# Kernel tuning notes

Hardware: AMD Instinct MI355X
Metric: run time of the kernel (lower is better)

## Reference

```python
import jax, jax.numpy as jnp
import numpy as np

D_MODEL = 512
NHEAD = 8
D_K = D_MODEL // NHEAD


def setup_inputs() -> dict:
    key = jax.random.key(0)
    ks = jax.random.split(key, 7)
    B, L = 4, 2048
    x = jax.random.normal(ks[0], (B, L, D_MODEL), dtype=jnp.float32)
    scale = 1.0 / np.sqrt(D_MODEL)
    Wq = jax.random.normal(ks[1], (D_MODEL, D_MODEL), dtype=jnp.float32) * scale
    Wk = jax.random.normal(ks[2], (D_MODEL, D_MODEL), dtype=jnp.float32) * scale
    Wv = jax.random.normal(ks[3], (D_MODEL, D_MODEL), dtype=jnp.float32) * scale
    Wo = jax.random.normal(ks[4], (D_MODEL, D_MODEL), dtype=jnp.float32) * scale
    wave_freq = jax.random.normal(ks[5], (NHEAD,), dtype=jnp.float32) * 0.1
    wave_phase = jnp.zeros((NHEAD,), dtype=jnp.float32)
    return {"x": x, "Wq": Wq, "Wk": Wk, "Wv": Wv, "Wo": Wo,
            "wave_freq": wave_freq, "wave_phase": wave_phase}


def reference(x, Wq, Wk, Wv, Wo, wave_freq, wave_phase):
    B, L, D = x.shape
    H, dk = NHEAD, D_K
    # nn.Linear(bias=False): y = x @ W.T
    q = (x @ Wq.T).reshape(B, L, H, dk).transpose(0, 2, 1, 3)  # (B,H,L,dk)
    k = (x @ Wk.T).reshape(B, L, H, dk).transpose(0, 2, 1, 3)
    v = (x @ Wv.T).reshape(B, L, H, dk).transpose(0, 2, 1, 3)
    pos = jnp.arange(L, dtype=x.dtype)  # (L,)
    two_pi = jnp.asarray(2.0 * np.pi, dtype=x.dtype)
    # wave: (H, L) -> broadcast as (1, H, 1, L) over key positions
    wave = jnp.cos(two_pi * wave_freq[:, None] * pos[None, :] + wave_phase[:, None])
    scores = jnp.einsum('bhqd,bhkd->bhqk', q, k) * (dk ** -0.5)
    scores = scores * wave[None, :, None, :]
    attn = jax.nn.softmax(scores, axis=-1)
    out = jnp.einsum('bhqk,bhkd->bhqd', attn, v)
    out = out.transpose(0, 2, 1, 3).reshape(B, L, D)
    return out @ Wo.T
```

## Files before the change

### kernel.cpp

```cpp
#include <hip/hip_runtime.h>
#include <math.h>

#define D_MODEL 512
#define NHEAD   8
#define DK      64
#define BATCH   4
#define SEQ     2048
#define MTOT    (BATCH*SEQ)
#define NXELEM  (MTOT*D_MODEL)
#define NWELEM  (4*D_MODEL*D_MODEL)

typedef _Float16 half8   __attribute__((ext_vector_type(8)));
typedef _Float16 half4_t __attribute__((ext_vector_type(4)));
typedef __fp16   fp16x2  __attribute__((ext_vector_type(2)));
typedef float    f32x4   __attribute__((ext_vector_type(4)));

#define MFMA32(a,b,c) __builtin_amdgcn_mfma_f32_16x16x32_f16((a),(b),(c),0,0,0)

#define WSCALE 0.18033688011117130f

__global__ __launch_bounds__(256) void cvt_kernel(
    const float* __restrict__ x,
    const float* __restrict__ Wq, const float* __restrict__ Wk,
    const float* __restrict__ Wv, const float* __restrict__ Wo,
    const float* __restrict__ wf, const float* __restrict__ wp,
    _Float16* __restrict__ Xh, _Float16* __restrict__ Wh,
    float* __restrict__ wtab)
{
    const int tid = blockIdx.x * 256 + threadIdx.x;
    int idx = tid * 4;
    if (idx < NXELEM + NWELEM) {
        const float* src; _Float16* dst; int off;
        if (idx < NXELEM) { src = x; dst = Xh; off = idx; }
        else {
            int r = idx - NXELEM;
            int sel = r >> 18;
            off = r & ((1 << 18) - 1);
            src = (sel == 0) ? Wq : (sel == 1) ? Wk : (sel == 2) ? Wv : Wo;
            dst = Wh + ((size_t)sel << 18);
        }
        float4 v = *(const float4*)(src + off);
        half4_t h;
        h[0] = (_Float16)v.x; h[1] = (_Float16)v.y;
        h[2] = (_Float16)v.z; h[3] = (_Float16)v.w;
        *(half4_t*)(dst + off) = h;
    } else {
        int widx = idx - (NXELEM + NWELEM);
        const int h = widx >> 11;
        const int pos0 = widx & 2047;
        const float f  = 6.28318530717958647692f * wf[h];
        const float ph = wp[h];
        float4 o;
        o.x = WSCALE * cosf(fmaf(f, (float)(pos0 + 0), ph));
        o.y = WSCALE * cosf(fmaf(f, (float)(pos0 + 1), ph));
        o.z = WSCALE * cosf(fmaf(f, (float)(pos0 + 2), ph));
        o.w = WSCALE * cosf(fmaf(f, (float)(pos0 + 3), ph));
        *(float4*)(wtab + widx) = o;
    }
}

__global__ __launch_bounds__(256) void qkv_mfma_kernel(
    const _Float16* __restrict__ Xh, const _Float16* __restrict__ Wh,
    const float* __restrict__ wtab,
    _Float16* __restrict__ Qh, _Float16* __restrict__ Kh,
    _Float16* __restrict__ Vth)
{
    __shared__ _Float16 As[128][72];
    __shared__ _Float16 Bs[192][72];

    const int t  = threadIdx.x;
    const int h  = blockIdx.x;
    const int m0 = blockIdx.y * 128;

    const int w = t >> 6, lane = t & 63, ln = lane & 15, quad = lane >> 4;
    const int ar = t >> 1, ac = (t & 1) * 32;
    const int br = t >> 2, bc = (t & 3) * 16;

    const _Float16* ag  = Xh + (size_t)(m0 + ar) * 512 + ac;
    const _Float16* bg0 = Wh + (size_t)(h * 64 + br) * 512 + bc;
    const _Float16* bg1 = bg0 + (1 << 18);
    const _Float16* bg2 = bg0 + (2 << 18);

    const f32x4 kZero = {0.f, 0.f, 0.f, 0.f};
    f32x4 acc[3][2][4];
    #pragma unroll
    for (int c = 0; c < 3; ++c)
        #pragma unroll
        for (int i = 0; i < 2; ++i)
            #pragma unroll
            for (int j = 0; j < 4; ++j) acc[c][i][j] = kZero;

    for (int k0 = 0; k0 < 512; k0 += 64) {
        half8 av[4], bv[6];
        #pragma unroll
        for (int i = 0; i < 4; ++i) av[i] = *(const half8*)(ag + k0 + i * 8);
        bv[0] = *(const half8*)(bg0 + k0);
        bv[1] = *(const half8*)(bg0 + k0 + 8);
        bv[2] = *(const half8*)(bg1 + k0);
        bv[3] = *(const half8*)(bg1 + k0 + 8);
        bv[4] = *(const half8*)(bg2 + k0);
        bv[5] = *(const half8*)(bg2 + k0 + 8);
        __syncthreads();
        #pragma unroll
        for (int i = 0; i < 4; ++i) *(half8*)&As[ar][ac + i * 8] = av[i];
        #pragma unroll
        for (int c = 0; c < 3; ++c) {
            *(half8*)&Bs[c * 64 + br][bc]     = bv[2 * c];
            *(half8*)&Bs[c * 64 + br][bc + 8] = bv[2 * c + 1];
        }
        __syncthreads();

        #pragma unroll
        for (int ks = 0; ks < 2; ++ks) {
            half8 af[2];
            #pragma unroll
            for (int mt = 0; mt < 2; ++mt)
                af[mt] = *(const half8*)&As[w * 32 + mt * 16 + ln][ks * 32 + quad * 8];
            #pragma unroll
            for (int c = 0; c < 3; ++c) {
                half8 bf[4];
                #pragma unroll
                for (int nt = 0; nt < 4; ++nt)
                    bf[nt] = *(const half8*)&Bs[c * 64 + nt * 16 + ln][ks * 32 + quad * 8];
                #pragma unroll
                for (int mt = 0; mt < 2; ++mt)
                    #pragma unroll
                    for (int nt = 0; nt < 4; ++nt)
                        acc[c][mt][nt] = MFMA32(af[mt], bf[nt], acc[c][mt][nt]);
            }
        }
    }

    const int b  = m0 >> 11;
    const int l0 = m0 & 2047;
    const float* wt = wtab + h * SEQ;

    #pragma unroll
    for (int which = 0; which < 2; ++which) {
        _Float16* dst = (which == 0 ? Qh : Kh) + (size_t)(b * NHEAD + h) * SEQ * DK;
        __syncthreads();
        _Float16* Ql = &As[0][0];
        #pragma unroll
        for (int mt = 0; mt < 2; ++mt)
            #pragma unroll
            for (int r = 0; r < 4; ++r) {
                const int lr = w * 32 + mt * 16 + quad * 4 + r;
                const float wv = (which == 1) ? wt[l0 + lr] : 1.0f;
                #pragma unroll
                for (int nt = 0; nt < 4; ++nt)
                    Ql[lr * 72 + nt * 16 + ln] = (_Float16)(acc[which][mt][nt][r] * wv);
            }
        __syncthreads();
        #pragma unroll
        for (int rr = 0; rr < 4; ++rr) {
            const int row = rr * 32 + (t >> 3);
            half8 v = *(const half8*)&Ql[row * 72 + (t & 7) * 8];
            *(half8*)(dst + (size_t)(l0 + row) * DK + (t & 7) * 8) = v;
        }
    }

    __syncthreads();
    _Float16* Vl = &As[0][0];
    #pragma unroll
    for (int nt = 0; nt < 4; ++nt) {
        half8 hv;
        #pragma unroll
        for (int mt = 0; mt < 2; ++mt)
            #pragma unroll
            for (int r = 0; r < 4; ++r)
                hv[mt * 4 + r] = (_Float16)acc[2][mt][nt][r];
        const int d = nt * 16 + ln;
        *(half8*)&Vl[d * 136 + w * 32 + quad * 8] = hv;
    }
    __syncthreads();
    _Float16* dst = Vth + (size_t)(b * NHEAD + h) * DK * SEQ;
    #pragma unroll
    for (int rr = 0; rr < 4; ++rr) {
        const int d = rr * 16 + (t >> 4);
        half8 v = *(const half8*)&Vl[d * 136 + (t & 15) * 8];
        *(half8*)(dst + (size_t)d * SEQ + l0 + (t & 15) * 8) = v;
    }
}

__global__ __launch_bounds__(512, 4) void attn_mfma_kernel(
    const _Float16* __restrict__ Qh, const _Float16* __restrict__ Kwh,
    const _Float16* __restrict__ Vth, _Float16* __restrict__ AOh)
{
    __shared__ _Float16 SM[2][4][64][72];

    const int bx = blockIdx.x;
    const int g8 = bx & 7;
    const int s  = bx >> 3;
    const int bh = g8 * 4 + (s >> 4);
    const int q0 = (s & 15) * 128;
    const int b = bh >> 3, h = bh & 7;

    const int t = threadIdx.x;
    const int w = t >> 6;
    const int wg = w & 3;
    const int half = w >> 2;
    const int lane = t & 63, ln = lane & 15, quad = lane >> 4;

    const _Float16* Qg = Qh + ((size_t)bh * SEQ + q0) * DK;
    const _Float16* Kg = Kwh + (size_t)bh * SEQ * DK;
    const _Float16* Vg = Vth + (size_t)bh * DK * SEQ;
    const int kbase = half * 1024;

    const int tl = t & 255;
    const int sr = tl >> 2, sc = (tl & 3) * 16;
    const int qr = t >> 2, qc = (t & 3) * 16;

    {
        const _Float16* qp = Qg + (size_t)qr * DK + qc;
        half8 qv0 = *(const half8*)(qp);
        half8 qv1 = *(const half8*)(qp + 8);
        const _Float16* kp = Kg + (size_t)(kbase + sr) * DK + sc;
        const _Float16* vp = Vg + (size_t)sr * SEQ + kbase + sc;
        half8 kv0 = *(const half8*)(kp);
        half8 kv1 = *(const half8*)(kp + 8);
        half8 vv0 = *(const half8*)(vp);
        half8 vv1 = *(const half8*)(vp + 8);
        _Float16* qd = &SM[1][2 + (qr >> 6)][qr & 63][qc];
        *(half8*)(qd)     = qv0;
        *(half8*)(qd + 8) = qv1;
        *(half8*)&SM[half][0][sr][sc]     = kv0;
        *(half8*)&SM[half][0][sr][sc + 8] = kv1;
        *(half8*)&SM[half][1][sr][sc]     = vv0;
        *(half8*)&SM[half][1][sr][sc + 8] = vv1;
    }
    __syncthreads();

    half8 qf[2][2];
    #pragma unroll
    for (int u = 0; u < 2; ++u) {
        const int row = wg * 32 + u * 16 + ln;
        const _Float16* qsrc = &SM[1][2 + (row >> 6)][row & 63][0];
        qf[u][0] = *(const half8*)(qsrc + quad * 8);
        qf[u][1] = *(const half8*)(qsrc + 32 + quad * 8);
    }

    const f32x4 kZero = {0.f, 0.f, 0.f, 0.f};
    f32x4 o[2][4];
    #pragma unroll
    for (int u = 0; u < 2; ++u)
        #pragma unroll
        for (int nt = 0; nt < 4; ++nt) o[u][nt] = kZero;
    float l_acc[2] = {0.f, 0.f};

    for (int kt = 0; kt < 16; ++kt) {
        const int cur = kt & 1;

        half8 pk0, pk1, pv0, pv1;
        const bool more = (kt + 1 < 16);
        if (more) {
            const _Float16* kp = Kg + (size_t)(kbase + (kt + 1) * 64 + sr) * DK + sc;
            const _Float16* vp = Vg + (size_t)sr * SEQ + kbase + (kt + 1) * 64 + sc;
            pk0 = *(const half8*)(kp);
            pk1 = *(const half8*)(kp + 8);
            pv0 = *(const half8*)(vp);
            pv1 = *(const half8*)(vp + 8);
        }

        const _Float16 (*Ks)[72] = SM[half][2 * cur];
        const _Float16 (*Vs)[72] = SM[half][2 * cur + 1];

        #pragma unroll
        for (int g = 0; g < 2; ++g) {
            half8 ka0 = *(const half8*)&Ks[(2 * g + 0) * 16 + ln][quad * 8];
            half8 ka1 = *(const half8*)&Ks[(2 * g + 0) * 16 + ln][32 + quad * 8];
            half8 kb0 = *(const half8*)&Ks[(2 * g + 1) * 16 + ln][quad * 8];
            half8 kb1 = *(const half8*)&Ks[(2 * g + 1) * 16 + ln][32 + quad * 8];
            half8 vf[4];
            #pragma unroll
            for (int nt = 0; nt < 4; ++nt)
                vf[nt] = *(const half8*)&Vs[nt * 16 + ln][g * 32 + quad * 8];

            #pragma unroll
            for (int u = 0; u < 2; ++u) {
                f32x4 s0 = MFMA32(ka0, qf[u][0], kZero);
                f32x4 s1 = MFMA32(kb0, qf[u][0], kZero);
                s0 = MFMA32(ka1, qf[u][1], s0);
                s1 = MFMA32(kb1, qf[u][1], s1);

                const float e00 = __builtin_amdgcn_exp2f(s0[0]);
                const float e01 = __builtin_amdgcn_exp2f(s0[1]);
                const float e02 = __builtin_amdgcn_exp2f(s0[2]);
                const float e03 = __builtin_amdgcn_exp2f(s0[3]);
                const float e10 = __builtin_amdgcn_exp2f(s1[0]);
                const float e11 = __builtin_amdgcn_exp2f(s1[1]);
                const float e12 = __builtin_amdgcn_exp2f(s1[2]);
                const float e13 = __builtin_amdgcn_exp2f(s1[3]);
                union { half8 v; fp16x2 h2[4]; } pu;
                pu.h2[0] = __builtin_amdgcn_cvt_pkrtz(e00, e01);
                pu.h2[1] = __builtin_amdgcn_cvt_pkrtz(e02, e03);
                pu.h2[2] = __builtin_amdgcn_cvt_pkrtz(e10, e11);
                pu.h2[3] = __builtin_amdgcn_cvt_pkrtz(e12, e13);
                l_acc[u] += ((e00 + e01) + (e02 + e03)) + ((e10 + e11) + (e12 + e13));

                #pragma unroll
                for (int nt = 0; nt < 4; ++nt)
                    o[u][nt] = MFMA32(pu.v, vf[nt], o[u][nt]);
            }
        }

        __syncthreads();
        if (more) {
            _Float16* kd = &SM[half][2 * (cur ^ 1)][sr][sc];
            _Float16* vd = &SM[half][2 * (cur ^ 1) + 1][sr][sc];
            *(half8*)(kd)     = pk0;
            *(half8*)(kd + 8) = pk1;
            *(half8*)(vd)     = pv0;
            *(half8*)(vd + 8) = pv1;
        }
        __syncthreads();
    }

    float* OP = (float*)&SM[0][0][0][0];
    const int idx = wg * 64 + lane;
    if (half == 1) {
        #pragma unroll
        for (int u = 0; u < 2; ++u)
            #pragma unroll
            for (int nt = 0; nt < 4; ++nt)
                #pragma unroll
                for (int r = 0; r < 4; ++r)
                    OP[((u * 4 + nt) * 4 + r) * 257 + idx] = o[u][nt][r];
        OP[32 * 257 + idx] = l_acc[0];
        OP[33 * 257 + idx] = l_acc[1];
    }
    __syncthreads();
    if (half == 0) {
        #pragma unroll
        for (int u = 0; u < 2; ++u)
            #pragma unroll
            for (int nt = 0; nt < 4; ++nt)
                #pragma unroll
                for (int r = 0; r < 4; ++r)
                    o[u][nt][r] += OP[((u * 4 + nt) * 4 + r) * 257 + idx];
        l_acc[0] += OP[32 * 257 + idx];
        l_acc[1] += OP[33 * 257 + idx];

        #pragma unroll
        for (int u = 0; u < 2; ++u) {
            l_acc[u] += __shfl_xor(l_acc[u], 16);
            l_acc[u] += __shfl_xor(l_acc[u], 32);
        }

        #pragma unroll
        for (int u = 0; u < 2; ++u)
            #pragma unroll
            for (int r = 0; r < 4; ++r) {
                const float lr  = __shfl(l_acc[u], quad * 4 + r, 16);
                const float inv = 1.0f / lr;
                const int lq = q0 + wg * 32 + u * 16 + quad * 4 + r;
                const size_t base = ((size_t)b * SEQ + lq) * D_MODEL + h * DK;
                #pragma unroll
                for (int nt = 0; nt < 4; ++nt)
                    AOh[base + nt * 16 + ln] = (_Float16)(o[u][nt][r] * inv);
            }
    }
}

__global__ __launch_bounds__(256) void out_mfma_kernel(
    const _Float16* __restrict__ AOh, const _Float16* __restrict__ Woh,
    float* __restrict__ out)
{
    __shared__ _Float16 As[128][72];
    __shared__ _Float16 Bs[64][72];

    const int t  = threadIdx.x;
    const int n0 = blockIdx.x * 64;
    const int m0 = blockIdx.y * 128;

    const int w = t >> 6, lane = t & 63, ln = lane & 15, quad = lane >> 4;
    const int ar = t >> 1, ac = (t & 1) * 32;
    const int br = t >> 2, bc = (t & 3) * 16;

    const _Float16* ag = AOh + (size_t)(m0 + ar) * 512 + ac;
    const _Float16* bg = Woh + (size_t)(n0 + br) * 512 + bc;

    const f32x4 kZero = {0.f, 0.f, 0.f, 0.f};
    f32x4 acc[2][4];
    #pragma unroll
    for (int i = 0; i < 2; ++i)
        #pragma unroll
        for (int j = 0; j < 4; ++j) acc[i][j] = kZero;

    for (int k0 = 0; k0 < 512; k0 += 64) {
        half8 av[4], bv[2];
        #pragma unroll
        for (int i = 0; i < 4; ++i) av[i] = *(const half8*)(ag + k0 + i * 8);
        #pragma unroll
        for (int i = 0; i < 2; ++i) bv[i] = *(const half8*)(bg + k0 + i * 8);
        __syncthreads();
        #pragma unroll
        for (int i = 0; i < 4; ++i) *(half8*)&As[ar][ac + i * 8] = av[i];
        #pragma unroll
        for (int i = 0; i < 2; ++i) *(half8*)&Bs[br][bc + i * 8] = bv[i];
        __syncthreads();

        #pragma unroll
        for (int ks = 0; ks < 2; ++ks) {
            half8 af[2], bf[4];
            #pragma unroll
            for (int mt = 0; mt < 2; ++mt)
                af[mt] = *(const half8*)&As[w * 32 + mt * 16 + ln][ks * 32 + quad * 8];
            #pragma unroll
            for (int nt = 0; nt < 4; ++nt)
                bf[nt] = *(const half8*)&Bs[nt * 16 + ln][ks * 32 + quad * 8];
            #pragma unroll
            for (int mt = 0; mt < 2; ++mt)
                #pragma unroll
                for (int nt = 0; nt < 4; ++nt)
                    acc[mt][nt] = MFMA32(af[mt], bf[nt], acc[mt][nt]);
        }
    }

    float* Os = (float*)&As[0][0];
    #pragma unroll
    for (int pass = 0; pass < 2; ++pass) {
        __syncthreads();
        if ((w >> 1) == pass) {
            const int rbase = (w & 1) * 32;
            #pragma unroll
            for (int mt = 0; mt < 2; ++mt)
                #pragma unroll
                for (int r = 0; r < 4; ++r) {
                    const int row = rbase + mt * 16 + quad * 4 + r;
                    #pragma unroll
                    for (int nt = 0; nt < 4; ++nt)
                        Os[row * 66 + nt * 16 + ln] = acc[mt][nt][r];
                }
        }
        __syncthreads();
        #pragma unroll
        for (int rr = 0; rr < 4; ++rr) {
            const int row = rr * 16 + (t >> 4);
            float4 v = *(const float4*)&Os[row * 66 + (t & 15) * 4];
            *(float4*)(out + (size_t)(m0 + pass * 64 + row) * 512 + n0 + (t & 15) * 4) = v;
        }
    }
}

extern "C" void kernel_launch(void* const* d_in, const int* in_sizes, int n_in,
                              void* d_out, int out_size, void* d_ws, size_t ws_size,
                              hipStream_t stream)
{
    (void)in_sizes; (void)n_in; (void)out_size; (void)ws_size;
    const float* x  = (const float*)d_in[0];
    const float* Wq = (const float*)d_in[1];
    const float* Wk = (const float*)d_in[2];
    const float* Wv = (const float*)d_in[3];
    const float* Wo = (const float*)d_in[4];
    const float* wf = (const float*)d_in[5];
    const float* wp = (const float*)d_in[6];
    float* out = (float*)d_out;

    const size_t NX = (size_t)MTOT * D_MODEL;
    _Float16* Xh  = (_Float16*)d_ws;
    _Float16* Wh  = Xh + NX;
    _Float16* Qh  = Wh + 4 * 262144;
    _Float16* Kh  = Qh + NX;
    _Float16* Vth = Kh + NX;
    _Float16* AOh = Vth + NX;
    float*    wtab = (float*)(AOh + NX);

    cvt_kernel<<<5136, 256, 0, stream>>>(x, Wq, Wk, Wv, Wo, wf, wp, Xh, Wh, wtab);

    dim3 g1(8, 64);
    qkv_mfma_kernel<<<g1, 256, 0, stream>>>(Xh, Wh, wtab, Qh, Kh, Vth);

    attn_mfma_kernel<<<512, 512, 0, stream>>>(Qh, Kh, Vth, AOh);

    dim3 g3(8, 64);
    out_mfma_kernel<<<g3, 256, 0, stream>>>(AOh, Wh + 3 * 262144, out);
}
```

Before: 155.7 us.

## Halve attention block to 256 threads with 64 query rows per wave

Attention blocks shrink from 8 to 4 waves. Each wave now owns 64 query rows instead of 32, and K/V tiles are 32 keys per step over 32 steps instead of 64 keys over 16 steps. The aim is more register-level reuse of each K/V fragment across query subtiles, and less shared memory per block so more blocks fit per CU. In exchange each wave needs more accumulator registers, which may cut occupancy, and there are twice as many loop iterations with two barriers each.

```diff
diff --git a/kernel.cpp b/kernel.cpp
--- a/kernel.cpp
+++ b/kernel.cpp
@@ -182,11 +182,15 @@
     }
 }
 
-__global__ __launch_bounds__(512, 4) void attn_mfma_kernel(
+#define KOFF(h,b) ((b) * 9728 + (h) * 4864)
+#define VOFF(h,b) (KOFF(h,b) + 2304)
+#define QOFF      9728
+
+__global__ __launch_bounds__(256) void attn_mfma_kernel(
     const _Float16* __restrict__ Qh, const _Float16* __restrict__ Kwh,
     const _Float16* __restrict__ Vth, _Float16* __restrict__ AOh)
 {
-    __shared__ _Float16 SM[2][4][64][72];
+    __shared__ _Float16 SMEM[19456];
 
     const int bx = blockIdx.x;
     const int g8 = bx & 7;
@@ -197,116 +201,120 @@
 
     const int t = threadIdx.x;
     const int w = t >> 6;
-    const int wg = w & 3;
-    const int half = w >> 2;
+    const int wg = w & 1;
+    const int ch = w >> 1;
     const int lane = t & 63, ln = lane & 15, quad = lane >> 4;
 
     const _Float16* Qg = Qh + ((size_t)bh * SEQ + q0) * DK;
     const _Float16* Kg = Kwh + (size_t)bh * SEQ * DK;
     const _Float16* Vg = Vth + (size_t)bh * DK * SEQ;
-    const int kbase = half * 1024;
-
-    const int tl = t & 255;
-    const int sr = tl >> 2, sc = (tl & 3) * 16;
-    const int qr = t >> 2, qc = (t & 3) * 16;
+    const int kbase = (t >> 7) * 1024;
+
+    const int tl  = t & 127;
+    const int skr = tl >> 2, skc = (tl & 3) * 16;
+    const int svr = tl >> 1, svc = (tl & 1) * 16;
 
     {
+        const int qr = t >> 1, qc = (t & 1) * 32;
         const _Float16* qp = Qg + (size_t)qr * DK + qc;
-        half8 qv0 = *(const half8*)(qp);
-        half8 qv1 = *(const half8*)(qp + 8);
-        const _Float16* kp = Kg + (size_t)(kbase + sr) * DK + sc;
-        const _Float16* vp = Vg + (size_t)sr * SEQ + kbase + sc;
+        half8 q0v = *(const half8*)(qp);
+        half8 q1v = *(const half8*)(qp + 8);
+        half8 q2v = *(const half8*)(qp + 16);
+        half8 q3v = *(const half8*)(qp + 24);
+        const _Float16* kp = Kg + (size_t)(kbase + skr) * DK + skc;
+        const _Float16* vp = Vg + (size_t)svr * SEQ + kbase + svc;
         half8 kv0 = *(const half8*)(kp);
         half8 kv1 = *(const half8*)(kp + 8);
         half8 vv0 = *(const half8*)(vp);
         half8 vv1 = *(const half8*)(vp + 8);
-        _Float16* qd = &SM[1][2 + (qr >> 6)][qr & 63][qc];
-        *(half8*)(qd)     = qv0;
-        *(half8*)(qd + 8) = qv1;
-        *(half8*)&SM[half][0][sr][sc]     = kv0;
-        *(half8*)&SM[half][0][sr][sc + 8] = kv1;
-        *(half8*)&SM[half][1][sr][sc]     = vv0;
-        *(half8*)&SM[half][1][sr][sc + 8] = vv1;
+        _Float16* qd = &SMEM[QOFF + qr * 64 + qc];
+        *(half8*)(qd)      = q0v;
+        *(half8*)(qd + 8)  = q1v;
+        *(half8*)(qd + 16) = q2v;
+        *(half8*)(qd + 24) = q3v;
+        _Float16* kd = &SMEM[KOFF(t >> 7, 0) + skr * 72 + skc];
+        _Float16* vd = &SMEM[VOFF(t >> 7, 0) + svr * 40 + svc];
+        *(half8*)(kd)     = kv0;
+        *(half8*)(kd + 8) = kv1;
+        *(half8*)(vd)     = vv0;
+        *(half8*)(vd + 8) = vv1;
     }
     __syncthreads();
 
-    half8 qf[2][2];
-    #pragma unroll
-    for (int u = 0; u < 2; ++u) {
-        const int row = wg * 32 + u * 16 + ln;
-        const _Float16* qsrc = &SM[1][2 + (row >> 6)][row & 63][0];
+    half8 qf[4][2];
+    #pragma unroll
+    for (int u = 0; u < 4; ++u) {
+        const _Float16* qsrc = &SMEM[QOFF + (wg * 64 + u * 16 + ln) * 64];
         qf[u][0] = *(const half8*)(qsrc + quad * 8);
         qf[u][1] = *(const half8*)(qsrc + 32 + quad * 8);
     }
+    __syncthreads();
 
     const f32x4 kZero = {0.f, 0.f, 0.f, 0.f};
-    f32x4 o[2][4];
-    #pragma unroll
-    for (int u = 0; u < 2; ++u)
+    f32x4 o[4][4];
+    #pragma unroll
+    for (int u = 0; u < 4; ++u)
         #pragma unroll
         for (int nt = 0; nt < 4; ++nt) o[u][nt] = kZero;
-    float l_acc[2] = {0.f, 0.f};
-
-    for (int kt = 0; kt < 16; ++kt) {
+    float l_acc[4] = {0.f, 0.f, 0.f, 0.f};
+
+    for (int kt = 0; kt < 32; ++kt) {
         const int cur = kt & 1;
 
         half8 pk0, pk1, pv0, pv1;
-        const bool more = (kt + 1 < 16);
+        const bool more = (kt + 1 < 32);
         if (more) {
-            const _Float16* kp = Kg + (size_t)(kbase + (kt + 1) * 64 + sr) * DK + sc;
-            const _Float16* vp = Vg + (size_t)sr * SEQ + kbase + (kt + 1) * 64 + sc;
+            const _Float16* kp = Kg + (size_t)(kbase + (kt + 1) * 32 + skr) * DK + skc;
+            const _Float16* vp = Vg + (size_t)svr * SEQ + kbase + (kt + 1) * 32 + svc;
             pk0 = *(const half8*)(kp);
             pk1 = *(const half8*)(kp + 8);
             pv0 = *(const half8*)(vp);
             pv1 = *(const half8*)(vp + 8);
         }
 
-        const _Float16 (*Ks)[72] = SM[half][2 * cur];
-        const _Float16 (*Vs)[72] = SM[half][2 * cur + 1];
-
-        #pragma unroll
-        for (int g = 0; g < 2; ++g) {
-            half8 ka0 = *(const half8*)&Ks[(2 * g + 0) * 16 + ln][quad * 8];
-            half8 ka1 = *(const half8*)&Ks[(2 * g + 0) * 16 + ln][32 + quad * 8];
-            half8 kb0 = *(const half8*)&Ks[(2 * g + 1) * 16 + ln][quad * 8];
-            half8 kb1 = *(const half8*)&Ks[(2 * g + 1) * 16 + ln][32 + quad * 8];
-            half8 vf[4];
+        const _Float16* Ks = &SMEM[KOFF(ch, cur)];
+        const _Float16* Vs = &SMEM[VOFF(ch, cur)];
+
+        half8 ka0 = *(const half8*)&Ks[(ln)      * 72 + quad * 8];
+        half8 ka1 = *(const half8*)&Ks[(ln)      * 72 + 32 + quad * 8];
+        half8 kb0 = *(const half8*)&Ks[(16 + ln) * 72 + quad * 8];
+        half8 kb1 = *(const half8*)&Ks[(16 + ln) * 72 + 32 + quad * 8];
+        half8 vf[4];
+        #pragma unroll
+        for (int nt = 0; nt < 4; ++nt)
+            vf[nt] = *(const half8*)&Vs[(nt * 16 + ln) * 40 + quad * 8];
+
+        #pragma unroll
+        for (int u = 0; u < 4; ++u) {
+            f32x4 s0 = MFMA32(ka0, qf[u][0], kZero);
+            f32x4 s1 = MFMA32(kb0, qf[u][0], kZero);
+            s0 = MFMA32(ka1, qf[u][1], s0);
+            s1 = MFMA32(kb1, qf[u][1], s1);
+
+            const float e00 = __builtin_amdgcn_exp2f(s0[0]);
+            const float e01 = __builtin_amdgcn_exp2f(s0[1]);
+            const float e02 = __builtin_amdgcn_exp2f(s0[2]);
+            const float e03 = __builtin_amdgcn_exp2f(s0[3]);
+            const float e10 = __builtin_amdgcn_exp2f(s1[0]);
+            const float e11 = __builtin_amdgcn_exp2f(s1[1]);
+            const float e12 = __builtin_amdgcn_exp2f(s1[2]);
+            const float e13 = __builtin_amdgcn_exp2f(s1[3]);
+            union { half8 v; fp16x2 h2[4]; } pu;
+            pu.h2[0] = __builtin_amdgcn_cvt_pkrtz(e00, e01);
+            pu.h2[1] = __builtin_amdgcn_cvt_pkrtz(e02, e03);
+            pu.h2[2] = __builtin_amdgcn_cvt_pkrtz(e10, e11);
+            pu.h2[3] = __builtin_amdgcn_cvt_pkrtz(e12, e13);
+            l_acc[u] += ((e00 + e01) + (e02 + e03)) + ((e10 + e11) + (e12 + e13));
+
             #pragma unroll
             for (int nt = 0; nt < 4; ++nt)
-                vf[nt] = *(const half8*)&Vs[nt * 16 + ln][g * 32 + quad * 8];
-
-            #pragma unroll
-            for (int u = 0; u < 2; ++u) {
-                f32x4 s0 = MFMA32(ka0, qf[u][0], kZero);
-                f32x4 s1 = MFMA32(kb0, qf[u][0], kZero);
-                s0 = MFMA32(ka1, qf[u][1], s0);
-                s1 = MFMA32(kb1, qf[u][1], s1);
-
-                const float e00 = __builtin_amdgcn_exp2f(s0[0]);
-                const float e01 = __builtin_amdgcn_exp2f(s0[1]);
-                const float e02 = __builtin_amdgcn_exp2f(s0[2]);
-                const float e03 = __builtin_amdgcn_exp2f(s0[3]);
-                const float e10 = __builtin_amdgcn_exp2f(s1[0]);
-                const float e11 = __builtin_amdgcn_exp2f(s1[1]);
-                const float e12 = __builtin_amdgcn_exp2f(s1[2]);
-                const float e13 = __builtin_amdgcn_exp2f(s1[3]);
-                union { half8 v; fp16x2 h2[4]; } pu;
-                pu.h2[0] = __builtin_amdgcn_cvt_pkrtz(e00, e01);
-                pu.h2[1] = __builtin_amdgcn_cvt_pkrtz(e02, e03);
-                pu.h2[2] = __builtin_amdgcn_cvt_pkrtz(e10, e11);
-                pu.h2[3] = __builtin_amdgcn_cvt_pkrtz(e12, e13);
-                l_acc[u] += ((e00 + e01) + (e02 + e03)) + ((e10 + e11) + (e12 + e13));
-
-                #pragma unroll
-                for (int nt = 0; nt < 4; ++nt)
-                    o[u][nt] = MFMA32(pu.v, vf[nt], o[u][nt]);
-            }
+                o[u][nt] = MFMA32(pu.v, vf[nt], o[u][nt]);
         }
 
         __syncthreads();
         if (more) {
-            _Float16* kd = &SM[half][2 * (cur ^ 1)][sr][sc];
-            _Float16* vd = &SM[half][2 * (cur ^ 1) + 1][sr][sc];
+            _Float16* kd = &SMEM[KOFF(t >> 7, cur ^ 1) + skr * 72 + skc];
+            _Float16* vd = &SMEM[VOFF(t >> 7, cur ^ 1) + svr * 40 + svc];
             *(half8*)(kd)     = pk0;
             *(half8*)(kd + 8) = pk1;
             *(half8*)(vd)     = pv0;
@@ -315,44 +323,44 @@
         __syncthreads();
     }
 
-    float* OP = (float*)&SM[0][0][0][0];
+    float* OP = (float*)&SMEM[0];
     const int idx = wg * 64 + lane;
-    if (half == 1) {
-        #pragma unroll
-        for (int u = 0; u < 2; ++u)
+    if (ch == 1) {
+        #pragma unroll
+        for (int u = 0; u < 4; ++u) {
             #pragma unroll
             for (int nt = 0; nt < 4; ++nt)
                 #pragma unroll
                 for (int r = 0; r < 4; ++r)
-                    OP[((u * 4 + nt) * 4 + r) * 257 + idx] = o[u][nt][r];
-        OP[32 * 257 + idx] = l_acc[0];
-        OP[33 * 257 + idx] = l_acc[1];
+                    OP[((u * 4 + nt) * 4 + r) * 129 + idx] = o[u][nt][r];
+            OP[(64 + u) * 129 + idx] = l_acc[u];
+        }
     }
     __syncthreads();
-    if (half == 0) {
-        #pragma unroll
-        for (int u = 0; u < 2; ++u)
+    if (ch == 0) {
+        #pragma unroll
+        for (int u = 0; u < 4; ++u) {
             #pragma unroll
             for (int nt = 0; nt < 4; ++nt)
                 #pragma unroll
                 for (int r = 0; r < 4; ++r)
-                    o[u][nt][r] += OP[((u * 4 + nt) * 4 + r) * 257 + idx];
-        l_acc[0] += OP[32 * 257 + idx];
-        l_acc[1] += OP[33 * 257 + idx];
-
-        #pragma unroll
-        for (int u = 0; u < 2; ++u) {
+                    o[u][nt][r] += OP[((u * 4 + nt) * 4 + r) * 129 + idx];
+            l_acc[u] += OP[(64 + u) * 129 + idx];
+        }
+
+        #pragma unroll
+        for (int u = 0; u < 4; ++u) {
             l_acc[u] += __shfl_xor(l_acc[u], 16);
             l_acc[u] += __shfl_xor(l_acc[u], 32);
         }
 
         #pragma unroll
-        for (int u = 0; u < 2; ++u)
+        for (int u = 0; u < 4; ++u)
             #pragma unroll
             for (int r = 0; r < 4; ++r) {
                 const float lr  = __shfl(l_acc[u], quad * 4 + r, 16);
                 const float inv = 1.0f / lr;
-                const int lq = q0 + wg * 32 + u * 16 + quad * 4 + r;
+                const int lq = q0 + wg * 64 + u * 16 + quad * 4 + r;
                 const size_t base = ((size_t)b * SEQ + lq) * D_MODEL + h * DK;
                 #pragma unroll
                 for (int nt = 0; nt < 4; ++nt)
@@ -470,7 +478,7 @@
     dim3 g1(8, 64);
     qkv_mfma_kernel<<<g1, 256, 0, stream>>>(Xh, Wh, wtab, Qh, Kh, Vth);
 
-    attn_mfma_kernel<<<512, 512, 0, stream>>>(Qh, Kh, Vth, AOh);
+    attn_mfma_kernel<<<512, 256, 0, stream>>>(Qh, Kh, Vth, AOh);
 
     dim3 g3(8, 64);
     out_mfma_kernel<<<g3, 256, 0, stream>>>(AOh, Wh + 3 * 262144, out);
```

Measured after the change: 169.4 us. 1.09x slower.
